# Kernel tuning notes

Hardware: AMD Instinct MI355X
Metric: run time of the kernel (lower is better)

Reference implementation:

```python
import jax, jax.numpy as jnp
import numpy as np

B, T, D, H, C = 256, 512, 64, 512, 1

def setup_inputs() -> dict:
    key = jax.random.key(0)
    ks = jax.random.split(key, 12)
    return {
        "x": jax.random.normal(ks[0], (B, T, D), jnp.float32),
        "w_ih_mu": jax.random.normal(ks[1], (D, 4 * H), jnp.float32) * 0.1,
        "w_ih_rho": jax.random.normal(ks[2], (D, 4 * H), jnp.float32) - 6.0,
        "eps_ih": jax.random.normal(ks[3], (D, 4 * H), jnp.float32),
        "w_hh_mu": jax.random.normal(ks[4], (H, 4 * H), jnp.float32) * 0.1,
        "w_hh_rho": jax.random.normal(ks[5], (H, 4 * H), jnp.float32) - 6.0,
        "eps_hh": jax.random.normal(ks[6], (H, 4 * H), jnp.float32),
        "b_mu": jax.random.normal(ks[7], (4 * H,), jnp.float32) * 0.1,
        "b_rho": jax.random.normal(ks[8], (4 * H,), jnp.float32) - 6.0,
        "eps_b": jax.random.normal(ks[9], (4 * H,), jnp.float32),
        "lin_w": jax.random.normal(ks[10], (C, H), jnp.float32) * 0.04,
        "lin_b": jax.random.normal(ks[11], (C,), jnp.float32) * 0.04,
    }

def _sample(mu, rho, eps):
    # blitz reparameterization: sigma = log1p(exp(rho))
    return mu + jnp.log1p(jnp.exp(rho)) * eps

def reference(x, w_ih_mu, w_ih_rho, eps_ih, w_hh_mu, w_hh_rho, eps_hh,
              b_mu, b_rho, eps_b, lin_w, lin_b):
    w_ih = _sample(w_ih_mu, w_ih_rho, eps_ih)
    w_hh = _sample(w_hh_mu, w_hh_rho, eps_hh)
    b = _sample(b_mu, b_rho, eps_b)

    # precompute input projections for all timesteps: [T, B, 4H]
    x_proj = jnp.einsum('btd,dg->tbg', x, w_ih) + b

    def step(carry, xp_t):
        h, c = carry
        gates = xp_t + h @ w_hh                      # [B, 4H]
        i, f, g, o = jnp.split(gates, 4, axis=-1)
        i = jax.nn.sigmoid(i)
        f = jax.nn.sigmoid(f)
        g = jnp.tanh(g)
        o = jax.nn.sigmoid(o)
        c = f * c + i * g
        h = o * jnp.tanh(c)
        return (h, c), None

    h0 = jnp.zeros((x.shape[0], w_hh.shape[0]), x.dtype)
    (h_last, _), _ = jax.lax.scan(step, (h0, h0), x_proj)
    # original takes outputs[:, -1, :] == last hidden state, then Linear
    return h_last @ lin_w.T + lin_b
```

## Files before the change

kernel.cpp:

```cpp
#include <hip/hip_runtime.h>

typedef unsigned short u16;
typedef unsigned long long u64;
typedef short v8s __attribute__((ext_vector_type(8)));
typedef float v4f __attribute__((ext_vector_type(4)));
typedef unsigned v2u __attribute__((ext_vector_type(2)));

#define Bb 256
#define Tt 512
#define Dd 64
#define Hh 512
#define G4 2048

#define NGROUP 16
#define NCHUNK 16
#define BT 16
#define HC 32
#define NCOL 128

#define WHH_S 520
#define WIH_S 72
#define SMEM_BYTES (NCOL*WHH_S*2 + NCOL*WIH_S*2)

#define MFMA(a,b,c) __builtin_amdgcn_mfma_f32_16x16x32_bf16((a),(b),(c),0,0,0)

__device__ __forceinline__ u16 f2bf(float f) {
  unsigned u = __float_as_uint(f);
  unsigned r = (u + 0x7fffu + ((u >> 16) & 1u)) >> 16;
  return (u16)r;
}
__device__ __forceinline__ float bf2f(u16 v) {
  return __uint_as_float(((unsigned)v) << 16);
}
__device__ __forceinline__ float sigm(float x) { return 1.0f / (1.0f + __expf(-x)); }
__device__ __forceinline__ float tanh_f(float x) {
  float a = fabsf(x);
  float e = __expf(-2.0f * a);
  float r = (1.0f - e) / (1.0f + e);
  return copysignf(r, x);
}
__device__ __forceinline__ float softplus_f(float x) { return log1pf(__expf(x)); }

__global__ void k_prep(const float* __restrict__ x, u16* __restrict__ x_bf,
                       unsigned* __restrict__ flags)
{
  if (blockIdx.x < 2) {
    int i = blockIdx.x * 256 + threadIdx.x;
    if (i < NGROUP * NCHUNK * 2) flags[i] = 0u;
  }
  const int N4 = Tt * Bb * Dd / 4;
  int stride = gridDim.x * blockDim.x;
  for (int i = blockIdx.x * blockDim.x + threadIdx.x; i < N4; i += stride) {
    int idx = i * 4;
    int t = idx >> 14;
    int rem = idx & 16383;
    int b = rem >> 6;
    int d = rem & 63;
    float4 v = *(const float4*)(x + (size_t)b * (Tt * Dd) + t * Dd + d);
    unsigned lo = (unsigned)f2bf(v.x) | ((unsigned)f2bf(v.y) << 16);
    unsigned hi = (unsigned)f2bf(v.z) | ((unsigned)f2bf(v.w) << 16);
    *(uint2*)(x_bf + idx) = make_uint2(lo, hi);
  }
}

__global__ __launch_bounds__(128, 1) void lstm_main(
    const float* __restrict__ whh_mu, const float* __restrict__ whh_rho, const float* __restrict__ whh_eps,
    const float* __restrict__ wih_mu, const float* __restrict__ wih_rho, const float* __restrict__ wih_eps,
    const float* __restrict__ b_mu,  const float* __restrict__ b_rho,  const float* __restrict__ b_eps,
    const u16* __restrict__ x_bf, u16* __restrict__ h_buf, unsigned* __restrict__ flags)
{
  extern __shared__ char smem[];
  u16* w_hh_lds = (u16*)smem;
  u16* w_ih_lds = w_hh_lds + NCOL * WHH_S;

  const int tid   = threadIdx.x;
  const int g     = blockIdx.x & 15;
  const int chunk = blockIdx.x >> 4;
  const int b0    = g * BT;
  const int j0    = chunk * HC;

  {
    const int lc = tid;
    const int gcol = (lc >> 5) * Hh + j0 + (lc & 31);
    #pragma unroll 4
    for (int k = 0; k < Hh; ++k) {
      int gi = k * G4 + gcol;
      float w = whh_mu[gi] + softplus_f(whh_rho[gi]) * whh_eps[gi];
      w_hh_lds[lc * WHH_S + k] = f2bf(w);
    }
    #pragma unroll 4
    for (int k = 0; k < Dd; ++k) {
      int gi = k * G4 + gcol;
      float w = wih_mu[gi] + softplus_f(wih_rho[gi]) * wih_eps[gi];
      w_ih_lds[lc * WIH_S + k] = f2bf(w);
    }
  }

  const int lane = tid & 63;
  const int wv   = tid >> 6;
  const int ln   = lane & 15;
  const int q    = lane >> 4;
  const int ko   = q * 8;

  const u16* WhP[4]; const u16* WxP[4];
  #pragma unroll
  for (int gt = 0; gt < 4; ++gt) {
    int rt = gt * 2 + wv;
    WhP[gt] = w_hh_lds + (rt * 16 + ln) * WHH_S + ko;
    WxP[gt] = w_ih_lds + (rt * 16 + ln) * WIH_S + ko;
  }

  const int bat = b0 + ln;

  float bs[4][4];
  #pragma unroll
  for (int gt = 0; gt < 4; ++gt)
    #pragma unroll
    for (int r = 0; r < 4; ++r) {
      int colg = gt * Hh + j0 + wv * 16 + q * 4 + r;
      bs[gt][r] = b_mu[colg] + softplus_f(b_rho[colg]) * b_eps[colg];
    }

  float cc[4] = {0.f, 0.f, 0.f, 0.f};
  unsigned* const fgrp2 = flags + g * (NCHUNK * 2);
  const unsigned* fp2 = fgrp2 + (lane & 31);
  __syncthreads();

  for (int t = 0; t < Tt; ++t) {
    v4f ac0 = {0.f,0.f,0.f,0.f}, ac1 = {0.f,0.f,0.f,0.f};
    v4f ac2 = {0.f,0.f,0.f,0.f}, ac3 = {0.f,0.f,0.f,0.f};

    {
      const u16* xb = x_bf + (size_t)t * (Bb * Dd) + bat * Dd + ko;
      #pragma unroll
      for (int ks = 0; ks < 2; ++ks) {
        v8s xf = *(const v8s*)(xb + ks * 32);
        ac0 = MFMA(*(const v8s*)(WxP[0] + ks * 32), xf, ac0);
        ac1 = MFMA(*(const v8s*)(WxP[1] + ks * 32), xf, ac1);
        ac2 = MFMA(*(const v8s*)(WxP[2] + ks * 32), xf, ac2);
        ac3 = MFMA(*(const v8s*)(WxP[3] + ks * 32), xf, ac3);
      }
    }

    if (t > 0) {
      const u16* hb = h_buf + (t & 1) * (Bb * Hh) + bat * Hh + ko;
      unsigned done = 0, todo = 0;
      v8s buf[16];
      for (;;) {
        unsigned pv = 0;
        bool needPoll = (done | todo) != 0xFFFFu;
        if (needPoll) {
          asm volatile("global_load_dword %0, %1, off sc0 sc1"
                       : "=v"(pv) : "v"(fp2));
        }
        #pragma unroll
        for (int c = 0; c < 16; ++c)
          if (todo & (1u << c)) {
            asm volatile("global_load_dwordx4 %0, %1, off offset:%c2 sc0 sc1"
                         : "=v"(buf[c]) : "v"(hb), "i"(c * 64));
          }
        asm volatile("s_waitcnt vmcnt(0)");
        if (needPoll) {
          asm volatile("" : "+v"(pv));
        }
        #pragma unroll
        for (int c = 0; c < 16; ++c)
          if (todo & (1u << c)) {
            asm volatile("" : "+v"(buf[c]));
            ac0 = MFMA(*(const v8s*)(WhP[0] + c * 32), buf[c], ac0);
            ac1 = MFMA(*(const v8s*)(WhP[1] + c * 32), buf[c], ac1);
            ac2 = MFMA(*(const v8s*)(WhP[2] + c * 32), buf[c], ac2);
            ac3 = MFMA(*(const v8s*)(WhP[3] + c * 32), buf[c], ac3);
          }
        done |= todo;
        if (done == 0xFFFFu) break;
        u64 bal = __ballot((int)(pv >= (unsigned)t));
        unsigned lo = (unsigned)bal;
        unsigned ready = lo & (lo >> 16) & 0xFFFFu;
        todo = ready & ~done;
      }
    }

    {
      u16 hv[4];
      #pragma unroll
      for (int r = 0; r < 4; ++r) {
        float ig = sigm  (ac0[r] + bs[0][r]);
        float fg = sigm  (ac1[r] + bs[1][r]);
        float gg = tanh_f(ac2[r] + bs[2][r]);
        float og = sigm  (ac3[r] + bs[3][r]);
        cc[r] = fg * cc[r] + ig * gg;
        hv[r] = f2bf(og * tanh_f(cc[r]));
      }
      v2u qv;
      qv[0] = (unsigned)hv[0] | ((unsigned)hv[1] << 16);
      qv[1] = (unsigned)hv[2] | ((unsigned)hv[3] << 16);
      u16* hp = h_buf + ((t + 1) & 1) * (Bb * Hh) + bat * Hh
              + j0 + wv * 16 + q * 4;
      asm volatile("global_store_dwordx2 %0, %1, off sc0 sc1"
                   :: "v"(hp), "v"(qv) : "memory");
    }

    asm volatile("s_waitcnt vmcnt(0)" ::: "memory");
    if (lane == 0) {
      unsigned tv = (unsigned)(t + 1);
      unsigned* fq = &fgrp2[wv * 16 + chunk];
      asm volatile("global_store_dword %0, %1, off sc0 sc1"
                   :: "v"(fq), "v"(tv) : "memory");
    }
  }
}

__global__ void k_out(const u16* __restrict__ h, const float* __restrict__ lw,
                      const float* __restrict__ lb, float* __restrict__ out)
{
  int b = blockIdx.x * 64 + threadIdx.x;
  if (b >= Bb) return;
  const u16* hr = h + b * Hh;
  float acc = 0.f;
  #pragma unroll 8
  for (int k = 0; k < Hh; ++k) acc += bf2f(hr[k]) * lw[k];
  out[b] = acc + lb[0];
}

extern "C" void kernel_launch(void* const* d_in, const int* in_sizes, int n_in,
                              void* d_out, int out_size, void* d_ws, size_t ws_size,
                              hipStream_t stream)
{
  (void)in_sizes; (void)n_in; (void)out_size; (void)ws_size;
  const float* x       = (const float*)d_in[0];
  const float* wih_mu  = (const float*)d_in[1];
  const float* wih_rho = (const float*)d_in[2];
  const float* wih_eps = (const float*)d_in[3];
  const float* whh_mu  = (const float*)d_in[4];
  const float* whh_rho = (const float*)d_in[5];
  const float* whh_eps = (const float*)d_in[6];
  const float* b_mu    = (const float*)d_in[7];
  const float* b_rho   = (const float*)d_in[8];
  const float* b_eps   = (const float*)d_in[9];
  const float* lin_w   = (const float*)d_in[10];
  const float* lin_b   = (const float*)d_in[11];
  float* out = (float*)d_out;

  u16* x_bf  = (u16*)d_ws;
  u16* h_buf = x_bf + (size_t)Tt * Bb * Dd;
  unsigned* flags = (unsigned*)(h_buf + 2 * Bb * Hh);

  k_prep<<<2048, 256, 0, stream>>>(x, x_bf, flags);

  hipFuncSetAttribute(reinterpret_cast<const void*>(lstm_main),
                      hipFuncAttributeMaxDynamicSharedMemorySize, SMEM_BYTES);
  lstm_main<<<NGROUP * NCHUNK, 128, SMEM_BYTES, stream>>>(
      whh_mu, whh_rho, whh_eps, wih_mu, wih_rho, wih_eps,
      b_mu, b_rho, b_eps, x_bf, h_buf, flags);

  k_out<<<(Bb + 63) / 64, 64, 0, stream>>>(h_buf, lin_w, lin_b, out);
}
```

Baseline: 2.466 ms.

## Replace flag handshake with sentinel-tagged hidden-state ring buffer

Drops the separate per-chunk flag array, whose use needed a store wait before each flag write plus a flag poll on every step. Consumers now load the hidden-state slices directly and treat a slice as ready once it holds no 0xFFFFFFFF sentinel words; producers re-arm a slot by writing sentinels into the slot consumed two steps earlier. The hidden-state buffer becomes a 4-slot ring so sentinel resets cannot race with readers. This relies on the sentinel bit pattern (a bf16 NaN) never appearing in real hidden states, and on the ordering of relaxed stores.

Result: no change. 2.500 ms (+1.4%).

```diff
diff --git a/kernel.cpp b/kernel.cpp
--- a/kernel.cpp
+++ b/kernel.cpp
@@ -5,6 +5,7 @@
 typedef short v8s __attribute__((ext_vector_type(8)));
 typedef float v4f __attribute__((ext_vector_type(4)));
 typedef unsigned v2u __attribute__((ext_vector_type(2)));
+typedef unsigned v4u __attribute__((ext_vector_type(4)));
 
 #define Bb 256
 #define Tt 512
@@ -23,6 +24,8 @@
 #define SMEM_BYTES (NCOL*WHH_S*2 + NCOL*WIH_S*2)
 
 #define MFMA(a,b,c) __builtin_amdgcn_mfma_f32_16x16x32_bf16((a),(b),(c),0,0,0)
+
+#define SENT 0xFFFFFFFFu
 
 __device__ __forceinline__ u16 f2bf(float f) {
   unsigned u = __float_as_uint(f);
@@ -42,15 +45,17 @@
 __device__ __forceinline__ float softplus_f(float x) { return log1pf(__expf(x)); }
 
 __global__ void k_prep(const float* __restrict__ x, u16* __restrict__ x_bf,
-                       unsigned* __restrict__ flags)
-{
-  if (blockIdx.x < 2) {
-    int i = blockIdx.x * 256 + threadIdx.x;
-    if (i < NGROUP * NCHUNK * 2) flags[i] = 0u;
-  }
+                       u16* __restrict__ h_buf)
+{
+  int stride = gridDim.x * blockDim.x;
+  int gid = blockIdx.x * blockDim.x + threadIdx.x;
+
+  const int NS = 4 * Bb * Hh / 8;
+  for (int i = gid; i < NS; i += stride)
+    ((uint4*)h_buf)[i] = make_uint4(~0u, ~0u, ~0u, ~0u);
+
   const int N4 = Tt * Bb * Dd / 4;
-  int stride = gridDim.x * blockDim.x;
-  for (int i = blockIdx.x * blockDim.x + threadIdx.x; i < N4; i += stride) {
+  for (int i = gid; i < N4; i += stride) {
     int idx = i * 4;
     int t = idx >> 14;
     int rem = idx & 16383;
@@ -67,7 +72,7 @@
     const float* __restrict__ whh_mu, const float* __restrict__ whh_rho, const float* __restrict__ whh_eps,
     const float* __restrict__ wih_mu, const float* __restrict__ wih_rho, const float* __restrict__ wih_eps,
     const float* __restrict__ b_mu,  const float* __restrict__ b_rho,  const float* __restrict__ b_eps,
-    const u16* __restrict__ x_bf, u16* __restrict__ h_buf, unsigned* __restrict__ flags)
+    const u16* __restrict__ x_bf, u16* __restrict__ h_buf)
 {
   extern __shared__ char smem[];
   u16* w_hh_lds = (u16*)smem;
@@ -122,8 +127,6 @@
     }
 
   float cc[4] = {0.f, 0.f, 0.f, 0.f};
-  unsigned* const fgrp2 = flags + g * (NCHUNK * 2);
-  const unsigned* fp2 = fgrp2 + (lane & 31);
   __syncthreads();
 
   for (int t = 0; t < Tt; ++t) {
@@ -143,42 +146,39 @@
     }
 
     if (t > 0) {
-      const u16* hb = h_buf + (t & 1) * (Bb * Hh) + bat * Hh + ko;
-      unsigned done = 0, todo = 0;
-      v8s buf[16];
-      for (;;) {
-        unsigned pv = 0;
-        bool needPoll = (done | todo) != 0xFFFFu;
-        if (needPoll) {
-          asm volatile("global_load_dword %0, %1, off sc0 sc1"
-                       : "=v"(pv) : "v"(fp2));
-        }
+      const u16* hb = h_buf + (size_t)(t & 3) * (Bb * Hh) + bat * Hh + ko;
+      unsigned done = 0;
+      v4u buf[16];
+      do {
         #pragma unroll
         for (int c = 0; c < 16; ++c)
-          if (todo & (1u << c)) {
+          if (!(done & (1u << c))) {
             asm volatile("global_load_dwordx4 %0, %1, off offset:%c2 sc0 sc1"
                          : "=v"(buf[c]) : "v"(hb), "i"(c * 64));
           }
         asm volatile("s_waitcnt vmcnt(0)");
-        if (needPoll) {
-          asm volatile("" : "+v"(pv));
-        }
+        unsigned ready = 0;
         #pragma unroll
         for (int c = 0; c < 16; ++c)
-          if (todo & (1u << c)) {
+          if (!(done & (1u << c))) {
             asm volatile("" : "+v"(buf[c]));
-            ac0 = MFMA(*(const v8s*)(WhP[0] + c * 32), buf[c], ac0);
-            ac1 = MFMA(*(const v8s*)(WhP[1] + c * 32), buf[c], ac1);
-            ac2 = MFMA(*(const v8s*)(WhP[2] + c * 32), buf[c], ac2);
-            ac3 = MFMA(*(const v8s*)(WhP[3] + c * 32), buf[c], ac3);
+            unsigned m0 = buf[c][0] > buf[c][1] ? buf[c][0] : buf[c][1];
+            unsigned m1 = buf[c][2] > buf[c][3] ? buf[c][2] : buf[c][3];
+            unsigned mx = m0 > m1 ? m0 : m1;
+            int ok = (mx != SENT);
+            if (__all(ok)) ready |= (1u << c);
           }
-        done |= todo;
-        if (done == 0xFFFFu) break;
-        u64 bal = __ballot((int)(pv >= (unsigned)t));
-        unsigned lo = (unsigned)bal;
-        unsigned ready = lo & (lo >> 16) & 0xFFFFu;
-        todo = ready & ~done;
-      }
+        #pragma unroll
+        for (int c = 0; c < 16; ++c)
+          if (ready & (1u << c)) {
+            v8s hf = __builtin_bit_cast(v8s, buf[c]);
+            ac0 = MFMA(*(const v8s*)(WhP[0] + c * 32), hf, ac0);
+            ac1 = MFMA(*(const v8s*)(WhP[1] + c * 32), hf, ac1);
+            ac2 = MFMA(*(const v8s*)(WhP[2] + c * 32), hf, ac2);
+            ac3 = MFMA(*(const v8s*)(WhP[3] + c * 32), hf, ac3);
+          }
+        done |= ready;
+      } while (done != 0xFFFFu);
     }
 
     {
@@ -195,18 +195,18 @@
       v2u qv;
       qv[0] = (unsigned)hv[0] | ((unsigned)hv[1] << 16);
       qv[1] = (unsigned)hv[2] | ((unsigned)hv[3] << 16);
-      u16* hp = h_buf + ((t + 1) & 1) * (Bb * Hh) + bat * Hh
+      u16* hp = h_buf + (size_t)((t + 1) & 3) * (Bb * Hh) + bat * Hh
               + j0 + wv * 16 + q * 4;
       asm volatile("global_store_dwordx2 %0, %1, off sc0 sc1"
                    :: "v"(hp), "v"(qv) : "memory");
     }
 
-    asm volatile("s_waitcnt vmcnt(0)" ::: "memory");
-    if (lane == 0) {
-      unsigned tv = (unsigned)(t + 1);
-      unsigned* fq = &fgrp2[wv * 16 + chunk];
-      asm volatile("global_store_dword %0, %1, off sc0 sc1"
-                   :: "v"(fq), "v"(tv) : "memory");
+    if (t > 0) {
+      u16* cp = h_buf + (size_t)((t - 1) & 3) * (Bb * Hh) + bat * Hh
+              + j0 + wv * 16 + q * 4;
+      v2u sv; sv[0] = SENT; sv[1] = SENT;
+      asm volatile("global_store_dwordx2 %0, %1, off sc0 sc1"
+                   :: "v"(cp), "v"(sv) : "memory");
     }
   }
 }
@@ -244,15 +244,14 @@
 
   u16* x_bf  = (u16*)d_ws;
   u16* h_buf = x_bf + (size_t)Tt * Bb * Dd;
-  unsigned* flags = (unsigned*)(h_buf + 2 * Bb * Hh);
-
-  k_prep<<<2048, 256, 0, stream>>>(x, x_bf, flags);
+
+  k_prep<<<2048, 256, 0, stream>>>(x, x_bf, h_buf);
 
   hipFuncSetAttribute(reinterpret_cast<const void*>(lstm_main),
                       hipFuncAttributeMaxDynamicSharedMemorySize, SMEM_BYTES);
   lstm_main<<<NGROUP * NCHUNK, 128, SMEM_BYTES, stream>>>(
       whh_mu, whh_rho, whh_eps, wih_mu, wih_rho, wih_eps,
-      b_mu, b_rho, b_eps, x_bf, h_buf, flags);
+      b_mu, b_rho, b_eps, x_bf, h_buf);
 
   k_out<<<(Bb + 63) / 64, 64, 0, stream>>>(h_buf, lin_w, lin_b, out);
 }
```
